# Kernel optimization log

Measured on AMD Instinct MI355X. Metric: run time of the kernel, lower is better.

Reference implementation:

```python
import jax, jax.numpy as jnp
import numpy as np

EMBED_DIM = 1024


def setup_inputs() -> dict:
    key = jax.random.key(0)
    ks = jax.random.split(key, 9)
    d = EMBED_DIM
    s = 1.0 / np.sqrt(d)
    x = jax.random.normal(ks[0], (4, 4096, d), dtype=jnp.float32)
    Wq = jax.random.normal(ks[1], (d, d), dtype=jnp.float32) * s
    bq = jax.random.normal(ks[2], (d,), dtype=jnp.float32) * 0.01
    Wk = jax.random.normal(ks[3], (d, d), dtype=jnp.float32) * s
    bk = jax.random.normal(ks[4], (d,), dtype=jnp.float32) * 0.01
    Wv = jax.random.normal(ks[5], (d, d), dtype=jnp.float32) * s
    bv = jax.random.normal(ks[6], (d,), dtype=jnp.float32) * 0.01
    Wo = jax.random.normal(ks[7], (d, d), dtype=jnp.float32) * s
    bo = jax.random.normal(ks[8], (d,), dtype=jnp.float32) * 0.01
    return {"x": x, "Wq": Wq, "bq": bq, "Wk": Wk, "bk": bk,
            "Wv": Wv, "bv": bv, "Wo": Wo, "bo": bo}


def reference(x, Wq, bq, Wk, bk, Wv, bv, Wo, bo):
    # x: [b, s, d]; single-head attention, scale = 1/sqrt(d)
    b, s, d = x.shape
    q = x @ Wq + bq
    k = x @ Wk + bk
    v = x @ Wv + bv
    scale = 1.0 / jnp.sqrt(jnp.asarray(d, x.dtype))
    scores = jnp.einsum('bqd,bkd->bqk', q, k) * scale  # [b, s, s]
    causal = jnp.tril(jnp.ones((s, s), dtype=bool))
    scores = jnp.where(causal, scores, jnp.asarray(-jnp.inf, scores.dtype))
    attn = jax.nn.softmax(scores, axis=-1)
    ctx = jnp.einsum('bqk,bkd->bqd', attn, v)
    return ctx @ Wo + bo
```

## Files before the change

kernel.cpp:

```cpp
#include <hip/hip_runtime.h>


typedef unsigned short u16;
typedef __attribute__((ext_vector_type(4))) unsigned short u16x4;
typedef __attribute__((ext_vector_type(8))) unsigned short u16x8;
typedef __attribute__((ext_vector_type(8))) __bf16 bf16x8;
typedef __attribute__((ext_vector_type(4))) float f32x4;

typedef const __attribute__((address_space(1))) void* as1cp;
typedef __attribute__((address_space(3))) void* as3p;

struct GemmPtrs {
  const u16* A[4];
  const u16* B[4];
  const float* bias[4];
  void* C[4];
};
struct TransPtrs {
  const void* in[4];
  u16* out[4];
};
struct SmPtrs {
  u16* P[4];
};

__device__ __forceinline__ u16 f2bf(float f) {
  union { float f; unsigned int i; } c; c.f = f;
  unsigned int r = c.i + 0x7fffu + ((c.i >> 16) & 1u);
  return (u16)(r >> 16);
}
__device__ __forceinline__ float bf2f(u16 u) {
  union { unsigned int i; float f; } c; c.i = ((unsigned int)u) << 16;
  return c.f;
}

__global__ __launch_bounds__(256) void cast_f32_bf16(const float* __restrict__ in,
                                                     u16* __restrict__ out, int n4) {
  int i = blockIdx.x * blockDim.x + threadIdx.x;
  if (i >= n4) return;
  float4 v = ((const float4*)in)[i];
  u16x4 u;
  u.x = f2bf(v.x); u.y = f2bf(v.y); u.z = f2bf(v.z); u.w = f2bf(v.w);
  ((u16x4*)out)[i] = u;
}

__global__ __launch_bounds__(256) void transpose_to_bf16(TransPtrs tp, int R, int C) {
  __shared__ u16 t[32][34];
  int z = blockIdx.z;
  int tx = threadIdx.x, ty = threadIdx.y;
  int c0 = blockIdx.x * 32, r0 = blockIdx.y * 32;
#pragma unroll
  for (int dy = 0; dy < 4; ++dy) {
    int r = r0 + ty + dy * 8;
    int c = c0 + tx;
    t[ty + dy * 8][tx] = f2bf(((const float*)tp.in[z])[(size_t)r * C + c]);
  }
  __syncthreads();
  u16* op = tp.out[z];
#pragma unroll
  for (int dy = 0; dy < 4; ++dy) {
    int a = ty + dy * 8;
    op[(size_t)(c0 + a) * R + r0 + tx] = t[tx][a];
  }
}

__global__ __launch_bounds__(256) void softmax_causal(SmPtrs sp) {
  int row = blockIdx.x;
  u16* P = sp.P[blockIdx.y];
  int tid = threadIdx.x;
  int lane = tid & 63, wv = tid >> 6;
  u16x8* prow = (u16x8*)(P + (size_t)row * 4096);
  int nch = (row >> 3) + 1;
  int fend = ((row >> 7) + 1) << 4;
  int c0 = tid, c1 = tid + 256;
  bool a0 = c0 < nch, a1 = c1 < nch;
  float vals[16];
  float lmax = -3.0e38f;
  if (a0) {
    u16x8 u = prow[c0];
#pragma unroll
    for (int e = 0; e < 8; ++e) {
      float f = (c0 * 8 + e <= row) ? bf2f(u[e]) : -3.0e38f;
      vals[e] = f; lmax = fmaxf(lmax, f);
    }
  } else {
#pragma unroll
    for (int e = 0; e < 8; ++e) vals[e] = -3.0e38f;
  }
  if (a1) {
    u16x8 u = prow[c1];
#pragma unroll
    for (int e = 0; e < 8; ++e) {
      float f = (c1 * 8 + e <= row) ? bf2f(u[e]) : -3.0e38f;
      vals[8 + e] = f; lmax = fmaxf(lmax, f);
    }
  } else {
#pragma unroll
    for (int e = 0; e < 8; ++e) vals[8 + e] = -3.0e38f;
  }
  __shared__ float red[8];
#pragma unroll
  for (int off = 32; off > 0; off >>= 1) lmax = fmaxf(lmax, __shfl_down(lmax, off, 64));
  if (lane == 0) red[wv] = lmax;
  __syncthreads();
  float m2 = fmaxf(fmaxf(red[0], red[1]), fmaxf(red[2], red[3]));
  float lsum = 0.f;
#pragma unroll
  for (int e = 0; e < 16; ++e) {
    float ev = __expf(vals[e] - m2);
    vals[e] = ev;
    lsum += ev;
  }
#pragma unroll
  for (int off = 32; off > 0; off >>= 1) lsum += __shfl_down(lsum, off, 64);
  if (lane == 0) red[4 + wv] = lsum;
  __syncthreads();
  float inv = 1.0f / (red[4] + red[5] + red[6] + red[7]);
  if (a0) {
    u16x8 u;
#pragma unroll
    for (int e = 0; e < 8; ++e) u[e] = f2bf(vals[e] * inv);
    prow[c0] = u;
  }
  if (a1) {
    u16x8 u;
#pragma unroll
    for (int e = 0; e < 8; ++e) u[e] = f2bf(vals[8 + e] * inv);
    prow[c1] = u;
  }
  u16x8 zz = (u16x8)(u16)0;
  for (int c = nch + tid; c < fend; c += 256) prow[c] = zz;
}

template <bool OUT_BF16, int BIAS_MODE, bool CAUSAL_SKIP, bool CAUSAL_KMAX>
__global__ __launch_bounds__(256) void gemm_bt(GemmPtrs p, int M, int N, int K,
                                               int ldb, float cscale) {
  __shared__ __align__(16) u16 As[2][128 * 64];
  __shared__ __align__(16) u16 Bs[2][128 * 64];
  int z = blockIdx.z;
  const u16* __restrict__ A = p.A[z];
  const u16* __restrict__ B = p.B[z];
  int bx = CAUSAL_KMAX ? (gridDim.x - 1 - blockIdx.x) : blockIdx.x;
  int tile_m = bx * 128;
  int tile_n = blockIdx.y * 128;
  if (CAUSAL_SKIP && tile_n >= tile_m + 128) return;

  int tid = threadIdx.x;
  int lane = tid & 63;
  int wv = tid >> 6;
  int wm = (wv >> 1) * 64;
  int wn = (wv & 1) * 64;
  int lrow = lane & 15;
  int lquad = lane >> 4;
  int srow = lane >> 3;
  int scol = ((lane & 7) ^ srow) * 8;
  int kmax = CAUSAL_KMAX ? min(K, tile_m + 128) : K;
  int niter = kmax >> 6;

  auto stage = [&](int k0, int sb) {
#pragma unroll
    for (int t = 0; t < 4; ++t) {
      int c = wv * 4 + t;
      int ar = c * 8 + srow;
      const u16* ga = A + (size_t)(tile_m + ar) * K + k0 + scol;
      __builtin_amdgcn_global_load_lds((as1cp)ga, (as3p)&As[sb][c * 512], 16, 0, 0);
      const u16* gb = B + (size_t)(tile_n + ar) * (size_t)ldb + k0 + scol;
      __builtin_amdgcn_global_load_lds((as1cp)gb, (as3p)&Bs[sb][c * 512], 16, 0, 0);
    }
  };

  f32x4 acc[4][4];
#pragma unroll
  for (int i = 0; i < 4; ++i)
#pragma unroll
    for (int j = 0; j < 4; ++j) acc[i][j] = (f32x4){0.f, 0.f, 0.f, 0.f};

  stage(0, 0);
  for (int it = 0; it < niter; ++it) {
    int cur = it & 1;
    if (it + 1 < niter) {
      stage((it + 1) << 6, cur ^ 1);
      asm volatile("s_waitcnt vmcnt(8)" ::: "memory");
    } else {
      asm volatile("s_waitcnt vmcnt(0)" ::: "memory");
    }
    asm volatile("s_barrier" ::: "memory");
#pragma unroll
    for (int ks = 0; ks < 64; ks += 32) {
      bf16x8 af[4], bg[4];
#pragma unroll
      for (int mt = 0; mt < 4; ++mt) {
        int r = wm + mt * 16 + lrow;
        int jb = (ks >> 3) + lquad;
        af[mt] = *(const bf16x8*)&As[cur][r * 64 + ((jb ^ (r & 7)) << 3)];
      }
#pragma unroll
      for (int nt = 0; nt < 4; ++nt) {
        int r = wn + nt * 16 + lrow;
        int jb = (ks >> 3) + lquad;
        bg[nt] = *(const bf16x8*)&Bs[cur][r * 64 + ((jb ^ (r & 7)) << 3)];
      }
#pragma unroll
      for (int mt = 0; mt < 4; ++mt)
#pragma unroll
        for (int nt = 0; nt < 4; ++nt)
          acc[mt][nt] = __builtin_amdgcn_mfma_f32_16x16x32_bf16(af[mt], bg[nt], acc[mt][nt], 0, 0, 0);
    }
    asm volatile("s_barrier" ::: "memory");
  }

#pragma unroll
  for (int mt = 0; mt < 4; ++mt) {
#pragma unroll
    for (int reg = 0; reg < 4; ++reg) {
      int r = tile_m + wm + mt * 16 + lquad * 4 + reg;
      float rb = (BIAS_MODE == 2) ? p.bias[z][r] : 0.f;
#pragma unroll
      for (int nt = 0; nt < 4; ++nt) {
        int cidx = tile_n + wn + nt * 16 + lrow;
        float vvv = acc[mt][nt][reg] * cscale + rb;
        if (BIAS_MODE == 1) vvv += p.bias[z][cidx];
        if (OUT_BF16) ((u16*)p.C[z])[(size_t)r * N + cidx] = f2bf(vvv);
        else          ((float*)p.C[z])[(size_t)r * N + cidx] = vvv;
      }
    }
  }
}

extern "C" void kernel_launch(void* const* d_in, const int* in_sizes, int n_in,
                              void* d_out, int out_size, void* d_ws, size_t ws_size,
                              hipStream_t stream) {
  const float* x  = (const float*)d_in[0];
  const float* Wq = (const float*)d_in[1];
  const float* bq = (const float*)d_in[2];
  const float* Wk = (const float*)d_in[3];
  const float* bk = (const float*)d_in[4];
  const float* Wv = (const float*)d_in[5];
  const float* bv = (const float*)d_in[6];
  const float* Wo = (const float*)d_in[7];
  const float* bo = (const float*)d_in[8];

  const int S = 4096, D = 1024, BATCH = 4;
  const size_t XE = (size_t)BATCH * S * D;
  const size_t BSE = (size_t)S * D;

  char* ws = (char*)d_ws;
  u16* xb  = (u16*)(ws + 0);
  u16* q   = (u16*)(ws + 33554432);
  u16* k   = (u16*)(ws + 67108864);
  u16* vT  = (u16*)(ws + 100663296);
  u16* ctx = (u16*)(ws + 134217728);
  u16* wqT = (u16*)(ws + 167772160);
  u16* wkT = wqT + 1048576;
  u16* wvT = wkT + 1048576;
  u16* woT = wvT + 1048576;
  u16* attn2 = (u16*)(ws + 176160768);
  u16* attn0 = (u16*)d_out;
  u16* attn1 = attn0 + (size_t)S * S;
  u16* attn3 = xb;
  u16* attn[4] = {attn0, attn1, attn2, attn3};

  cast_f32_bf16<<<(int)(XE / 4 / 256), 256, 0, stream>>>(x, xb, (int)(XE / 4));

  {
    TransPtrs tp = {{Wq, Wk, Wv, Wo}, {wqT, wkT, wvT, woT}};
    transpose_to_bf16<<<dim3(32, 32, 4), dim3(32, 8), 0, stream>>>(tp, D, D);
  }
  {
    GemmPtrs gp = {{xb, xb, xb, xb}, {wqT, wkT, wqT, wqT},
                   {bq, bk, bq, bq}, {q, k, q, q}};
    gemm_bt<true, 1, false, false><<<dim3(128, 8, 2), 256, 0, stream>>>(
        gp, 16384, D, D, D, 1.0f);
  }
  {
    GemmPtrs gp = {{wvT, wvT, wvT, wvT}, {xb, xb, xb, xb},
                   {bv, bv, bv, bv}, {vT, vT, vT, vT}};
    gemm_bt<true, 2, false, false><<<dim3(8, 128, 1), 256, 0, stream>>>(
        gp, D, 16384, D, D, 1.0f);
  }
  {
    GemmPtrs gp = {{q, q + BSE, q + 2 * BSE, q + 3 * BSE},
                   {k, k + BSE, k + 2 * BSE, k + 3 * BSE},
                   {nullptr, nullptr, nullptr, nullptr},
                   {attn[0], attn[1], attn[2], attn[3]}};
    gemm_bt<true, 0, true, false><<<dim3(32, 32, 4), 256, 0, stream>>>(
        gp, S, S, D, D, 0.03125f);
  }
  {
    SmPtrs sp = {{attn[0], attn[1], attn[2], attn[3]}};
    softmax_causal<<<dim3(S, 4), 256, 0, stream>>>(sp);
  }
  {
    GemmPtrs gp = {{attn[0], attn[1], attn[2], attn[3]},
                   {vT, vT + S, vT + 2 * S, vT + 3 * S},
                   {nullptr, nullptr, nullptr, nullptr},
                   {ctx, ctx + BSE, ctx + 2 * BSE, ctx + 3 * BSE}};
    gemm_bt<true, 0, false, true><<<dim3(32, 8, 4), 256, 0, stream>>>(
        gp, S, D, S, BATCH * S, 1.0f);
  }
  {
    GemmPtrs gp = {{ctx, ctx, ctx, ctx}, {woT, woT, woT, woT},
                   {bo, bo, bo, bo}, {d_out, d_out, d_out, d_out}};
    gemm_bt<false, 1, false, false><<<dim3(128, 8, 1), 256, 0, stream>>>(
        gp, 16384, D, D, D, 1.0f);
  }
}
```

Measured before the change: 627.8 us.

## Replace grid GEMMs with persistent 512-block kernels with cross-tile prefetch pipelining

Rewrites the tiled bf16 GEMM as a persistent kernel launched with 512 blocks. Each block walks a fixed list of tiles and keeps prefetching the next tile's K-slices across tile boundaries, so the double-buffered pipeline does not drain between tiles. For causal QK^T, triangular tiles are enumerated directly and balanced across blocks. For PV, long and short rows are paired per block so every block does 66 K-iterations. The V projection is merged into the QKV GEMM, followed by a separate bf16 transpose of V. This aims to remove load imbalance, tail effects and pipeline refill costs, at the price of an extra transpose pass and more complex index math.

```diff
diff --git a/kernel.cpp b/kernel.cpp
--- a/kernel.cpp
+++ b/kernel.cpp
@@ -44,6 +44,7 @@
   ((u16x4*)out)[i] = u;
 }
 
+template <bool IN_F32>
 __global__ __launch_bounds__(256) void transpose_to_bf16(TransPtrs tp, int R, int C) {
   __shared__ u16 t[32][34];
   int z = blockIdx.z;
@@ -53,7 +54,10 @@
   for (int dy = 0; dy < 4; ++dy) {
     int r = r0 + ty + dy * 8;
     int c = c0 + tx;
-    t[ty + dy * 8][tx] = f2bf(((const float*)tp.in[z])[(size_t)r * C + c]);
+    u16 hv;
+    if (IN_F32) hv = f2bf(((const float*)tp.in[z])[(size_t)r * C + c]);
+    else        hv = ((const u16*)tp.in[z])[(size_t)r * C + c];
+    t[ty + dy * 8][tx] = hv;
   }
   __syncthreads();
   u16* op = tp.out[z];
@@ -132,39 +136,53 @@
   for (int c = nch + tid; c < fend; c += 256) prow[c] = zz;
 }
 
-template <bool OUT_BF16, int BIAS_MODE, bool CAUSAL_SKIP, bool CAUSAL_KMAX>
-__global__ __launch_bounds__(256) void gemm_bt(GemmPtrs p, int M, int N, int K,
-                                               int ldb, float cscale) {
+template <int MODE, bool OUT_BF16, bool HAS_BIAS, int MAXSLOT>
+__global__ __launch_bounds__(256) void gemm_persist(GemmPtrs p, int K, int ldb, int N,
+                                                    float cscale) {
   __shared__ __align__(16) u16 As[2][128 * 64];
   __shared__ __align__(16) u16 Bs[2][128 * 64];
-  int z = blockIdx.z;
-  const u16* __restrict__ A = p.A[z];
-  const u16* __restrict__ B = p.B[z];
-  int bx = CAUSAL_KMAX ? (gridDim.x - 1 - blockIdx.x) : blockIdx.x;
-  int tile_m = bx * 128;
-  int tile_n = blockIdx.y * 128;
-  if (CAUSAL_SKIP && tile_n >= tile_m + 128) return;
-
-  int tid = threadIdx.x;
-  int lane = tid & 63;
-  int wv = tid >> 6;
-  int wm = (wv >> 1) * 64;
-  int wn = (wv & 1) * 64;
-  int lrow = lane & 15;
-  int lquad = lane >> 4;
-  int srow = lane >> 3;
-  int scol = ((lane & 7) ^ srow) * 8;
-  int kmax = CAUSAL_KMAX ? min(K, tile_m + 128) : K;
-  int niter = kmax >> 6;
-
-  auto stage = [&](int k0, int sb) {
-#pragma unroll
-    for (int t = 0; t < 4; ++t) {
-      int c = wv * 4 + t;
+  int b = blockIdx.x;
+  int tid = threadIdx.x, lane = tid & 63, wv = tid >> 6;
+  int wm = (wv >> 1) * 64, wn = (wv & 1) * 64;
+  int lrow = lane & 15, lquad = lane >> 4;
+  int srow = lane >> 3, scol = ((lane & 7) ^ srow) * 8;
+
+  struct TP { const u16* A; const u16* B; int niter, tm, tn, z; };
+  auto tileOf = [&](int s) {
+    TP t;
+    if (MODE == 0) {
+      int tt = s * 512 + b; t.z = tt >> 10; int m = tt & 1023;
+      t.tm = (m >> 3) << 7; t.tn = (m & 7) << 7; t.niter = K >> 6;
+    } else if (MODE == 1) {
+      int tt = (s < 4) ? s * 512 + b : 2048 + b;
+      t.z = tt / 528; int L = tt - t.z * 528;
+      int i = (int)((__fsqrt_rn(8.f * (float)L + 1.f) - 1.f) * 0.5f);
+      while ((i + 1) * (i + 2) / 2 <= L) ++i;
+      while (i * (i + 1) / 2 > L) --i;
+      t.tm = i << 7; t.tn = (L - ((i * (i + 1)) >> 1)) << 7; t.niter = K >> 6;
+    } else if (MODE == 2) {
+      int g = b >> 5, w = b & 31; t.z = w >> 3;
+      int i = (s == 0) ? 31 - g : g;
+      t.tm = i << 7; t.tn = (w & 7) << 7; t.niter = (i + 1) * 2;
+    } else {
+      int tt = s * 512 + b; t.z = 0;
+      t.tm = (tt >> 3) << 7; t.tn = (tt & 7) << 7; t.niter = K >> 6;
+    }
+    t.A = p.A[t.z] + (size_t)t.tm * K;
+    t.B = p.B[t.z] + (size_t)t.tn * ldb;
+    return t;
+  };
+  int nslot = (MODE == 1) ? (b < 64 ? 5 : 4) : MAXSLOT;
+  int total = (MODE == 2) ? 66 : nslot * (K >> 6);
+
+  auto stage = [&](const TP& t, int k0, int sb) {
+#pragma unroll
+    for (int tt = 0; tt < 4; ++tt) {
+      int c = wv * 4 + tt;
       int ar = c * 8 + srow;
-      const u16* ga = A + (size_t)(tile_m + ar) * K + k0 + scol;
+      const u16* ga = t.A + (size_t)ar * K + k0 + scol;
       __builtin_amdgcn_global_load_lds((as1cp)ga, (as3p)&As[sb][c * 512], 16, 0, 0);
-      const u16* gb = B + (size_t)(tile_n + ar) * (size_t)ldb + k0 + scol;
+      const u16* gb = t.B + (size_t)ar * ldb + k0 + scol;
       __builtin_amdgcn_global_load_lds((as1cp)gb, (as3p)&Bs[sb][c * 512], 16, 0, 0);
     }
   };
@@ -175,11 +193,47 @@
 #pragma unroll
     for (int j = 0; j < 4; ++j) acc[i][j] = (f32x4){0.f, 0.f, 0.f, 0.f};
 
-  stage(0, 0);
-  for (int it = 0; it < niter; ++it) {
-    int cur = it & 1;
-    if (it + 1 < niter) {
-      stage((it + 1) << 6, cur ^ 1);
+  auto epi = [&](const TP& t) {
+    const float* bias = HAS_BIAS ? p.bias[t.z] : nullptr;
+#pragma unroll
+    for (int mt = 0; mt < 4; ++mt) {
+#pragma unroll
+      for (int reg = 0; reg < 4; ++reg) {
+        int r = t.tm + wm + mt * 16 + lquad * 4 + reg;
+#pragma unroll
+        for (int nt = 0; nt < 4; ++nt) {
+          int cidx = t.tn + wn + nt * 16 + lrow;
+          float vvv = acc[mt][nt][reg] * cscale;
+          if (HAS_BIAS) vvv += bias[cidx];
+          if (OUT_BF16) ((u16*)p.C[t.z])[(size_t)r * N + cidx] = f2bf(vvv);
+          else          ((float*)p.C[t.z])[(size_t)r * N + cidx] = vvv;
+        }
+      }
+    }
+#pragma unroll
+    for (int i = 0; i < 4; ++i)
+#pragma unroll
+      for (int j = 0; j < 4; ++j) acc[i][j] = (f32x4){0.f, 0.f, 0.f, 0.f};
+  };
+
+  TP st = tileOf(0);
+  int stk = 0, sslot = 0;
+  auto adv = [&]() {
+    if (++stk == st.niter) {
+      stk = 0;
+      if (++sslot < nslot) st = tileOf(sslot);
+    }
+  };
+  TP ct = st;
+  int cit = 0, cslot = 0;
+
+  stage(st, 0, 0);
+  adv();
+  for (int it = 0; it < total; ++it) {
+    int cb = it & 1;
+    if (it + 1 < total) {
+      stage(st, stk << 6, cb ^ 1);
+      adv();
       asm volatile("s_waitcnt vmcnt(8)" ::: "memory");
     } else {
       asm volatile("s_waitcnt vmcnt(0)" ::: "memory");
@@ -192,13 +246,13 @@
       for (int mt = 0; mt < 4; ++mt) {
         int r = wm + mt * 16 + lrow;
         int jb = (ks >> 3) + lquad;
-        af[mt] = *(const bf16x8*)&As[cur][r * 64 + ((jb ^ (r & 7)) << 3)];
+        af[mt] = *(const bf16x8*)&As[cb][r * 64 + ((jb ^ (r & 7)) << 3)];
       }
 #pragma unroll
       for (int nt = 0; nt < 4; ++nt) {
         int r = wn + nt * 16 + lrow;
         int jb = (ks >> 3) + lquad;
-        bg[nt] = *(const bf16x8*)&Bs[cur][r * 64 + ((jb ^ (r & 7)) << 3)];
+        bg[nt] = *(const bf16x8*)&Bs[cb][r * 64 + ((jb ^ (r & 7)) << 3)];
       }
 #pragma unroll
       for (int mt = 0; mt < 4; ++mt)
@@ -207,22 +261,10 @@
           acc[mt][nt] = __builtin_amdgcn_mfma_f32_16x16x32_bf16(af[mt], bg[nt], acc[mt][nt], 0, 0, 0);
     }
     asm volatile("s_barrier" ::: "memory");
-  }
-
-#pragma unroll
-  for (int mt = 0; mt < 4; ++mt) {
-#pragma unroll
-    for (int reg = 0; reg < 4; ++reg) {
-      int r = tile_m + wm + mt * 16 + lquad * 4 + reg;
-      float rb = (BIAS_MODE == 2) ? p.bias[z][r] : 0.f;
-#pragma unroll
-      for (int nt = 0; nt < 4; ++nt) {
-        int cidx = tile_n + wn + nt * 16 + lrow;
-        float vvv = acc[mt][nt][reg] * cscale + rb;
-        if (BIAS_MODE == 1) vvv += p.bias[z][cidx];
-        if (OUT_BF16) ((u16*)p.C[z])[(size_t)r * N + cidx] = f2bf(vvv);
-        else          ((float*)p.C[z])[(size_t)r * N + cidx] = vvv;
-      }
+    if (++cit == ct.niter) {
+      epi(ct);
+      cit = 0;
+      if (++cslot < nslot) ct = tileOf(cslot);
     }
   }
 }
@@ -240,15 +282,15 @@
   const float* Wo = (const float*)d_in[7];
   const float* bo = (const float*)d_in[8];
 
-  const int S = 4096, D = 1024, BATCH = 4;
-  const size_t XE = (size_t)BATCH * S * D;
+  const int S = 4096, D = 1024;
+  const size_t XE = (size_t)4 * S * D;
   const size_t BSE = (size_t)S * D;
 
   char* ws = (char*)d_ws;
   u16* xb  = (u16*)(ws + 0);
   u16* q   = (u16*)(ws + 33554432);
   u16* k   = (u16*)(ws + 67108864);
-  u16* vT  = (u16*)(ws + 100663296);
+  u16* v   = (u16*)(ws + 100663296);
   u16* ctx = (u16*)(ws + 134217728);
   u16* wqT = (u16*)(ws + 167772160);
   u16* wkT = wqT + 1048576;
@@ -257,34 +299,31 @@
   u16* attn2 = (u16*)(ws + 176160768);
   u16* attn0 = (u16*)d_out;
   u16* attn1 = attn0 + (size_t)S * S;
-  u16* attn3 = xb;
+  u16* attn3 = v;
+  u16* vT = xb;
   u16* attn[4] = {attn0, attn1, attn2, attn3};
 
   cast_f32_bf16<<<(int)(XE / 4 / 256), 256, 0, stream>>>(x, xb, (int)(XE / 4));
-
   {
     TransPtrs tp = {{Wq, Wk, Wv, Wo}, {wqT, wkT, wvT, woT}};
-    transpose_to_bf16<<<dim3(32, 32, 4), dim3(32, 8), 0, stream>>>(tp, D, D);
-  }
-  {
-    GemmPtrs gp = {{xb, xb, xb, xb}, {wqT, wkT, wqT, wqT},
-                   {bq, bk, bq, bq}, {q, k, q, q}};
-    gemm_bt<true, 1, false, false><<<dim3(128, 8, 2), 256, 0, stream>>>(
-        gp, 16384, D, D, D, 1.0f);
-  }
-  {
-    GemmPtrs gp = {{wvT, wvT, wvT, wvT}, {xb, xb, xb, xb},
-                   {bv, bv, bv, bv}, {vT, vT, vT, vT}};
-    gemm_bt<true, 2, false, false><<<dim3(8, 128, 1), 256, 0, stream>>>(
-        gp, D, 16384, D, D, 1.0f);
+    transpose_to_bf16<true><<<dim3(32, 32, 4), dim3(32, 8), 0, stream>>>(tp, D, D);
+  }
+  {
+    GemmPtrs gp = {{xb, xb, xb, xb}, {wqT, wkT, wvT, wqT},
+                   {bq, bk, bv, bq}, {q, k, v, q}};
+    gemm_persist<0, true, true, 6><<<512, 256, 0, stream>>>(gp, D, D, D, 1.0f);
+  }
+  {
+    TransPtrs tp = {{v, v + BSE, v + 2 * BSE, v + 3 * BSE},
+                    {vT, vT + BSE, vT + 2 * BSE, vT + 3 * BSE}};
+    transpose_to_bf16<false><<<dim3(D / 32, S / 32, 4), dim3(32, 8), 0, stream>>>(tp, S, D);
   }
   {
     GemmPtrs gp = {{q, q + BSE, q + 2 * BSE, q + 3 * BSE},
                    {k, k + BSE, k + 2 * BSE, k + 3 * BSE},
                    {nullptr, nullptr, nullptr, nullptr},
                    {attn[0], attn[1], attn[2], attn[3]}};
-    gemm_bt<true, 0, true, false><<<dim3(32, 32, 4), 256, 0, stream>>>(
-        gp, S, S, D, D, 0.03125f);
+    gemm_persist<1, true, false, 5><<<512, 256, 0, stream>>>(gp, D, D, S, 0.03125f);
   }
   {
     SmPtrs sp = {{attn[0], attn[1], attn[2], attn[3]}};
@@ -292,16 +331,14 @@
   }
   {
     GemmPtrs gp = {{attn[0], attn[1], attn[2], attn[3]},
-                   {vT, vT + S, vT + 2 * S, vT + 3 * S},
+                   {vT, vT + BSE, vT + 2 * BSE, vT + 3 * BSE},
                    {nullptr, nullptr, nullptr, nullptr},
                    {ctx, ctx + BSE, ctx + 2 * BSE, ctx + 3 * BSE}};
-    gemm_bt<true, 0, false, true><<<dim3(32, 8, 4), 256, 0, stream>>>(
-        gp, S, D, S, BATCH * S, 1.0f);
+    gemm_persist<2, true, false, 2><<<512, 256, 0, stream>>>(gp, S, S, D, 1.0f);
   }
   {
     GemmPtrs gp = {{ctx, ctx, ctx, ctx}, {woT, woT, woT, woT},
                    {bo, bo, bo, bo}, {d_out, d_out, d_out, d_out}};
-    gemm_bt<false, 1, false, false><<<dim3(128, 8, 1), 256, 0, stream>>>(
-        gp, 16384, D, D, D, 1.0f);
-  }
-}
+    gemm_persist<3, false, true, 2><<<512, 256, 0, stream>>>(gp, D, D, D, 1.0f);
+  }
+}
```

Result: faster. 614.8 us (-2.1%).
